# Performance work log

Measured on AMD Instinct MI355X. Metric: run time of the kernel, lower is better.

Reference implementation:

```python
import jax, jax.numpy as jnp
import numpy as np

B, C, H, W, HID = 4, 32, 256, 256, 64
EPS = 1e-5


def setup_inputs() -> dict:
    key = jax.random.key(0)
    ks = jax.random.split(key, 8)
    s = 0.05
    return {
        "x": jax.random.normal(ks[0], (B, C, H, W), jnp.float32),
        "Wqkv": jax.random.normal(ks[1], (3 * C, C), jnp.float32) * s,   # Conv2d 1x1, no bias
        "W1": jax.random.normal(ks[2], (HID, C), jnp.float32) * s,       # Linear(C -> HID)
        "b1": jnp.zeros((HID,), jnp.float32),
        "ln_w": jnp.ones((HID,), jnp.float32),
        "ln_b": jnp.zeros((HID,), jnp.float32),
        "W2": jax.random.normal(ks[3], (C, HID), jnp.float32) * s,       # Linear(HID -> C)
        "b2": jnp.zeros((C,), jnp.float32),
        "Wg": jax.random.normal(ks[4], (C, C), jnp.float32) * s,         # gate Conv2d 1x1
        "bg": jnp.zeros((C,), jnp.float32),
    }


def _unfold3x3(t):
    # t: (b, c, h, w) -> (b, c, 9, h, w), zero-padded 3x3 neighbors,
    # neighbor order matches F.unfold row-major kernel order.
    b, c, h, w = t.shape
    tp = jnp.pad(t, ((0, 0), (0, 0), (1, 1), (1, 1)))
    return jnp.stack(
        [tp[:, :, dy:dy + h, dx:dx + w] for dy in range(3) for dx in range(3)],
        axis=2,
    )


def reference(x, Wqkv, W1, b1, ln_w, ln_b, W2, b2, Wg, bg):
    b, c, h, w = x.shape
    qkv = jnp.einsum('oc,bchw->bohw', Wqkv, x)
    q, k, v = jnp.split(qkv, 3, axis=1)

    k_un = _unfold3x3(k)  # (b, c, 9, h, w)
    v_un = _unfold3x3(v)

    # (b, h, w, 9, c)
    q_minus_k = jnp.transpose(q[:, :, None] - k_un, (0, 3, 4, 2, 1))

    hid = jnp.einsum('bhwnc,dc->bhwnd', q_minus_k, W1) + b1
    mean = hid.mean(-1, keepdims=True)
    std = jnp.sqrt(((hid - mean) ** 2).mean(-1, keepdims=True))  # unbiased=False
    hid = ln_w * ((hid - mean) / (std + EPS)) + ln_b
    hid = jax.nn.relu(hid)
    scores = jnp.einsum('bhwnd,cd->bhwnc', hid, W2) + b2

    attn = jax.nn.softmax(scores, axis=-2)  # over neighbor dim (9)
    neighbors_v = jnp.transpose(v_un, (0, 3, 4, 2, 1))  # (b, h, w, 9, c)
    weighted_v = jnp.sum(neighbors_v * attn, axis=3)     # (b, h, w, c)
    weighted_v = jnp.transpose(weighted_v, (0, 3, 1, 2)) # (b, c, h, w)

    base = jnp.einsum('oc,bchw->bohw', Wg, x) + bg[None, :, None, None]
    return weighted_v + base + x
```

## Files before the change

kernel.cpp:

```cpp
#include <hip/hip_runtime.h>


#define HWm 65536
#define NPIX 262144
#define PW 258
#define PHW 66564
#define LOG2E 1.44269504088896340736f

typedef __attribute__((ext_vector_type(8))) _Float16 half8;
typedef __attribute__((ext_vector_type(2))) _Float16 half2v;
typedef __attribute__((ext_vector_type(4))) float f32x4;

__device__ __forceinline__ unsigned pkh(float a, float b) {
    auto h = __builtin_amdgcn_cvt_pkrtz(a, b);
    return __builtin_bit_cast(unsigned, h);
}
__device__ __forceinline__ half2v h2(unsigned u) { return __builtin_bit_cast(half2v, u); }
__device__ __forceinline__ unsigned u2(half2v h) { return __builtin_bit_cast(unsigned, h); }

__global__ __launch_bounds__(256) void prep_kernel(
    const float* __restrict__ Wqkv, const float* __restrict__ W1,
    const float* __restrict__ W2, const float* __restrict__ b1v,
    const float* __restrict__ Wg, const float* __restrict__ bgv,
    const float* __restrict__ lnw, const float* __restrict__ lnb,
    float* __restrict__ Wk1, float* __restrict__ Wq1,
    unsigned* __restrict__ W2A, unsigned* __restrict__ waA,
    float* __restrict__ biasF, unsigned* __restrict__ beta2G)
{
    const int tid = threadIdx.x;
    for (int i = tid; i < 2048; i += 256) {
        const int d = i >> 5, c = i & 31;
        float aq = 0.f, ak = 0.f;
#pragma unroll
        for (int k = 0; k < 32; ++k) {
            const float w1 = W1[d * 32 + k];
            aq = fmaf(w1, Wqkv[k * 32 + c], aq);
            ak = fmaf(w1, Wqkv[(32 + k) * 32 + c], ak);
        }
        Wq1[i] = aq;
        Wk1[i] = ak;
    }
    for (int i = tid; i < 1024; i += 256) {
        const int w = i & 3;
        const int lane = (i >> 2) & 63;
        const int kb = (i >> 8) & 1;
        const int ct = (i >> 9) & 1;
        const int row = (lane & 15) + 16 * ct;
        const int k0 = kb * 32 + ((lane >> 4) & 3) * 8 + 2 * w;
        const float s0 = (fabsf(lnw[k0]) < 1e-8f) ? 0.f : lnw[k0] * LOG2E;
        const float s1 = (fabsf(lnw[k0 + 1]) < 1e-8f) ? 0.f : lnw[k0 + 1] * LOG2E;
        W2A[i] = pkh(W2[row * 64 + k0] * s0, W2[row * 64 + k0 + 1] * s1);
    }
    for (int i = tid; i < 32; i += 256) {
        const float w0 = lnw[2 * i], w1 = lnw[2 * i + 1];
        const float be0 = (fabsf(w0) < 1e-8f) ? 0.f : lnb[2 * i] / w0;
        const float be1 = (fabsf(w1) < 1e-8f) ? 0.f : lnb[2 * i + 1] / w1;
        beta2G[i] = pkh(be0, be1);
    }
    __syncthreads();
    for (int i = tid; i < 3072; i += 256) {
        const int t = i >> 8;
        const int l = (i >> 2) & 63;
        const int w2 = i & 3;
        const int row = 16 * t + (l & 15);
        const int k0 = ((l >> 4) & 3) * 8 + 2 * w2;
        float a0, a1;
        if (row < 64)        { a0 = Wk1[row * 32 + k0];            a1 = Wk1[row * 32 + k0 + 1]; }
        else if (row < 128)  { a0 = Wq1[(row - 64) * 32 + k0];     a1 = Wq1[(row - 64) * 32 + k0 + 1]; }
        else if (row < 160)  { a0 = Wqkv[(row - 64) * 32 + k0];    a1 = Wqkv[(row - 64) * 32 + k0 + 1]; }
        else {
            const int gr = row - 160;
            a0 = Wg[gr * 32 + k0]     + ((gr == k0)     ? 1.f : 0.f);
            a1 = Wg[gr * 32 + k0 + 1] + ((gr == k0 + 1) ? 1.f : 0.f);
        }
        waA[i] = pkh(a0, a1);
    }
    for (int i = tid; i < 3072; i += 256) {
        const int t = i >> 8;
        const int l = (i >> 2) & 63;
        const int r = i & 3;
        const int row = 16 * t + ((l >> 4) & 3) * 4 + r;
        float bv = 0.f;
        if (row >= 64 && row < 128) bv = b1v[row - 64];
        else if (row >= 160)        bv = bgv[row - 160];
        biasF[i] = bv;
    }
}

__global__ __launch_bounds__(256) void kv_kernel(
    const float* __restrict__ x, const half8* __restrict__ waA,
    const float4* __restrict__ biasF, unsigned* __restrict__ khP,
    unsigned* __restrict__ qhg, unsigned* __restrict__ vP,
    float* __restrict__ SkP, float* __restrict__ SqG,
    float* __restrict__ out)
{
    const int bid = blockIdx.x;
    const int tid = threadIdx.x;

    if (bid >= 1024) {
        const int t = (bid - 1024) * 256 + tid;
        if (t < 4112) {
            const int bb = t / 1028;
            const int rr = t - bb * 1028;
            int hh, ww;
            if (rr < 258)      { hh = 0;             ww = rr; }
            else if (rr < 516) { hh = 257;           ww = rr - 258; }
            else if (rr < 772) { hh = rr - 516 + 1;  ww = 0; }
            else               { hh = rr - 772 + 1;  ww = 257; }
            const size_t pixP = (size_t)bb * PHW + hh * PW + ww;
            uint4* kp = (uint4*)khP + pixP * 8;
            uint4* vp = (uint4*)vP + pixP * 4;
            const uint4 z = { 0u, 0u, 0u, 0u };
#pragma unroll
            for (int i = 0; i < 8; ++i) kp[i] = z;
#pragma unroll
            for (int i = 0; i < 4; ++i) vp[i] = z;
            SkP[pixP] = 0.f;
        }
        return;
    }

    __shared__ __align__(16) unsigned xT[256 * 16];

    const int b = bid >> 8;
    const int h = bid & 255;
    const int pix0 = bid * 256;
    const int rowP0 = b * PHW + (h + 1) * PW + 1;

    {
        const float* xp = x + (size_t)b * (32 * HWm) + h * 256 + tid;
        float xv[32];
#pragma unroll
        for (int c = 0; c < 32; ++c) xv[c] = xp[c * HWm];
        unsigned* myx = &xT[tid * 16];
#pragma unroll
        for (int cc = 0; cc < 4; ++cc) {
            uint4 u;
            u.x = pkh(xv[cc * 8 + 0], xv[cc * 8 + 1]);
            u.y = pkh(xv[cc * 8 + 2], xv[cc * 8 + 3]);
            u.z = pkh(xv[cc * 8 + 4], xv[cc * 8 + 5]);
            u.w = pkh(xv[cc * 8 + 6], xv[cc * 8 + 7]);
            *(uint4*)(myx + (((cc + tid) & 3) * 4)) = u;
        }
    }

    const int l = tid & 63;
    const int wid = tid >> 6;
    const int g = l >> 4;
    const int c15 = l & 15;

    half8 A[12];
    f32x4 bF[12];
#pragma unroll
    for (int t = 0; t < 12; ++t) {
        A[t] = waA[t * 64 + l];
        const float4 bv = biasF[t * 64 + l];
        bF[t][0] = bv.x; bF[t][1] = bv.y; bF[t][2] = bv.z; bF[t][3] = bv.w;
    }

#pragma unroll
    for (int pp = 0; pp < 4; ++pp) {
        const int pg = wid * 4 + pp;
        const int px = pg * 16 + c15;
        const half8 bfrag = *(const half8*)&xT[px * 16 + (((g + px) & 3) * 4)];

        f32x4 Ct[12];
#pragma unroll
        for (int t = 0; t < 12; ++t)
            Ct[t] = __builtin_amdgcn_mfma_f32_16x16x32_f16(A[t], bfrag, bF[t], 0, 0, 0);

        const size_t pixP = (size_t)(rowP0 + px);
        const int pixg = pix0 + px;

        float sk = 0.f;
        {
            char* krec = (char*)khP + pixP * 128 + g * 8;
#pragma unroll
            for (int t = 0; t < 4; ++t) {
                uint2 uu;
                uu.x = pkh(Ct[t][0], Ct[t][1]);
                uu.y = pkh(Ct[t][2], Ct[t][3]);
                *(uint2*)(krec + t * 32) = uu;
                sk += (Ct[t][0] + Ct[t][1]) + (Ct[t][2] + Ct[t][3]);
            }
        }
        float sq = 0.f;
        {
            char* qrec = (char*)qhg + (size_t)pixg * 128 + g * 8;
#pragma unroll
            for (int t = 4; t < 8; ++t) {
                uint2 uu;
                uu.x = pkh(Ct[t][0], Ct[t][1]);
                uu.y = pkh(Ct[t][2], Ct[t][3]);
                *(uint2*)(qrec + (t - 4) * 32) = uu;
                sq += (Ct[t][0] + Ct[t][1]) + (Ct[t][2] + Ct[t][3]);
            }
        }
        {
            char* vrec = (char*)vP + pixP * 64 + g * 8;
#pragma unroll
            for (int t = 8; t < 10; ++t) {
                uint2 uu;
                uu.x = pkh(Ct[t][0], Ct[t][1]);
                uu.y = pkh(Ct[t][2], Ct[t][3]);
                *(uint2*)(vrec + (t - 8) * 32) = uu;
            }
        }
        {
            float* op = out + (size_t)b * (32 * HWm) + h * 256 + px;
#pragma unroll
            for (int t = 10; t < 12; ++t) {
#pragma unroll
                for (int r = 0; r < 4; ++r)
                    op[(16 * (t - 10) + g * 4 + r) * HWm] = Ct[t][r];
            }
        }
        sk += __shfl_xor(sk, 16);
        sk += __shfl_xor(sk, 32);
        sq += __shfl_xor(sq, 16);
        sq += __shfl_xor(sq, 32);
        if (g == 0) {
            SkP[pixP] = sk;
            SqG[pixg] = sq;
        }
    }
}

__global__ __launch_bounds__(512) void attn_kernel(
    const unsigned* __restrict__ qhg, const unsigned* __restrict__ khP,
    const unsigned* __restrict__ vP, const half8* __restrict__ w2a,
    const float* __restrict__ SkP, const float* __restrict__ SqG,
    const unsigned* __restrict__ beta2G, float* __restrict__ out)
{
    __shared__ __align__(16) char mergeL[32768];

    const int tid = threadIdx.x;
    const int grp = tid >> 8;
    const int p = tid & 255;

    const int bid = blockIdx.x;
    const int swz = (bid & 7) * 128 + (bid >> 3);
    const int b = swz >> 8;
    const int trem = swz & 255;
    const int h0 = (trem >> 4) << 4;
    const int w0 = (trem & 15) << 4;

    const int l = tid & 63;
    const int lane15 = p & 15;
    const int q = (p >> 4) & 3;
    const int wrow = (p >> 6) & 3;
    const int gRow0 = wrow * 4;

    const int pixU0 = (b << 16) + ((h0 + gRow0) << 8) + (w0 + lane15);
    const int pixP0 = b * PHW + (h0 + gRow0 + 1) * PW + (w0 + lane15 + 1);

    uint4 qf[4][2];
    float Sq4[4];
#pragma unroll
    for (int gg = 0; gg < 4; ++gg) {
        const uint4* qr = (const uint4*)qhg + (size_t)(pixU0 + gg * 256) * 8;
        qf[gg][0] = qr[q];
        qf[gg][1] = qr[4 + q];
        Sq4[gg] = SqG[pixU0 + gg * 256];
    }

    half2v bet[2][4];
#pragma unroll
    for (int j = 0; j < 4; ++j) {
        bet[0][j] = h2(beta2G[q * 4 + j]);
        bet[1][j] = h2(beta2G[(4 + q) * 4 + j]);
    }

    const half8 a00 = w2a[0 * 64 + l];
    const half8 a01 = w2a[1 * 64 + l];
    const half8 a10 = w2a[2 * 64 + l];
    const half8 a11 = w2a[3 * 64 + l];

    half2v wv2[16], ssum2[16];
    const half2v zero2 = { (_Float16)0.f, (_Float16)0.f };
#pragma unroll
    for (int i = 0; i < 16; ++i) { wv2[i] = zero2; ssum2[i] = zero2; }

    const uint4* khP4 = (const uint4*)khP;
    const int vbase0 = b * PHW + (h0 + 1) * PW + (w0 + 1) + lane15;

    const int cnt = grp ? 5 : 4;
    int relOff = grp ? 0 : (-PW - 1);
    int m3 = grp ? 1 : 0;

#pragma unroll
    for (int nn = 0; nn < 5; ++nn) {
        if (nn >= cnt) break;

        float ss[4];
        half2v hd[4][2][4];
#pragma unroll
        for (int gg = 0; gg < 4; ++gg) {
            const int nofs = pixP0 + gg * PW + relOff;
            const uint4* kr = khP4 + (size_t)nofs * 8;
            const uint4 k0 = kr[q];
            const uint4 k1 = kr[4 + q];
            hd[gg][0][0] = h2(qf[gg][0].x) - h2(k0.x);
            hd[gg][0][1] = h2(qf[gg][0].y) - h2(k0.y);
            hd[gg][0][2] = h2(qf[gg][0].z) - h2(k0.z);
            hd[gg][0][3] = h2(qf[gg][0].w) - h2(k0.w);
            hd[gg][1][0] = h2(qf[gg][1].x) - h2(k1.x);
            hd[gg][1][1] = h2(qf[gg][1].y) - h2(k1.y);
            hd[gg][1][2] = h2(qf[gg][1].z) - h2(k1.z);
            hd[gg][1][3] = h2(qf[gg][1].w) - h2(k1.w);
            float s = 0.f;
#pragma unroll
            for (int c = 0; c < 2; ++c)
#pragma unroll
                for (int j = 0; j < 4; ++j)
                    s = __builtin_amdgcn_fdot2(hd[gg][c][j], hd[gg][c][j], s, false);
            ss[gg] = s;
        }
#pragma unroll
        for (int gg = 0; gg < 4; ++gg) {
            ss[gg] += __shfl_xor(ss[gg], 16);
            ss[gg] += __shfl_xor(ss[gg], 32);
        }

#pragma unroll
        for (int gg = 0; gg < 4; ++gg) {
            const float Sk = SkP[pixP0 + gg * PW + relOff];
            const float sum = Sq4[gg] - Sk;
            const float mean = sum * 0.015625f;
            float var = fmaf(-mean, mean, ss[gg] * 0.015625f);
            var = fmaxf(var, 0.f);
            const float inv = __builtin_amdgcn_rcpf(sqrtf(var) + 1e-5f);
            const float nmi = -mean * inv;
            const half2v inv2 = { (_Float16)inv, (_Float16)inv };
            const half2v nmi2 = { (_Float16)nmi, (_Float16)nmi };

            uint4 u0, u1;
            {
                unsigned uw[2][4];
#pragma unroll
                for (int c = 0; c < 2; ++c)
#pragma unroll
                    for (int j = 0; j < 4; ++j) {
                        half2v u = __builtin_elementwise_fma(hd[gg][c][j], inv2, nmi2 + bet[c][j]);
                        u = __builtin_elementwise_max(u, zero2);
                        uw[c][j] = u2(u);
                    }
                u0.x = uw[0][0]; u0.y = uw[0][1]; u0.z = uw[0][2]; u0.w = uw[0][3];
                u1.x = uw[1][0]; u1.y = uw[1][1]; u1.z = uw[1][2]; u1.w = uw[1][3];
            }
            const half8 B0 = __builtin_bit_cast(half8, u0);
            const half8 B1 = __builtin_bit_cast(half8, u1);

            const f32x4 z4 = { 0.f, 0.f, 0.f, 0.f };
            f32x4 acc0 = __builtin_amdgcn_mfma_f32_16x16x32_f16(a00, B0, z4, 0, 0, 0);
            acc0 = __builtin_amdgcn_mfma_f32_16x16x32_f16(a01, B1, acc0, 0, 0, 0);
            f32x4 acc1 = __builtin_amdgcn_mfma_f32_16x16x32_f16(a10, B0, z4, 0, 0, 0);
            acc1 = __builtin_amdgcn_mfma_f32_16x16x32_f16(a11, B1, acc1, 0, 0, 0);

            const int npP = vbase0 + (gRow0 + gg) * PW + relOff;
            const unsigned* vp = vP + (size_t)npP * 16;
            const uint2 vA = *(const uint2*)(vp + q * 2);
            const uint2 vB = *(const uint2*)(vp + 8 + q * 2);

            const half2v e01 = h2(pkh(__builtin_amdgcn_exp2f(acc0[0]), __builtin_amdgcn_exp2f(acc0[1])));
            const half2v e23 = h2(pkh(__builtin_amdgcn_exp2f(acc0[2]), __builtin_amdgcn_exp2f(acc0[3])));
            const half2v f01 = h2(pkh(__builtin_amdgcn_exp2f(acc1[0]), __builtin_amdgcn_exp2f(acc1[1])));
            const half2v f23 = h2(pkh(__builtin_amdgcn_exp2f(acc1[2]), __builtin_amdgcn_exp2f(acc1[3])));
            ssum2[gg * 4 + 0] += e01;
            ssum2[gg * 4 + 1] += e23;
            ssum2[gg * 4 + 2] += f01;
            ssum2[gg * 4 + 3] += f23;
            wv2[gg * 4 + 0] = __builtin_elementwise_fma(e01, h2(vA.x), wv2[gg * 4 + 0]);
            wv2[gg * 4 + 1] = __builtin_elementwise_fma(e23, h2(vA.y), wv2[gg * 4 + 1]);
            wv2[gg * 4 + 2] = __builtin_elementwise_fma(f01, h2(vB.x), wv2[gg * 4 + 2]);
            wv2[gg * 4 + 3] = __builtin_elementwise_fma(f23, h2(vB.y), wv2[gg * 4 + 3]);
        }

        const int step = (m3 == 2) ? (PW - 2) : 1;
        relOff += step;
        m3 = (m3 == 2) ? 0 : m3 + 1;
    }

    __syncthreads();
    if (grp == 1) {
#pragma unroll
        for (int j4 = 0; j4 < 4; ++j4) {
            uint4 o;
            o.x = u2(wv2[j4 * 4 + 0]); o.y = u2(wv2[j4 * 4 + 1]);
            o.z = u2(wv2[j4 * 4 + 2]); o.w = u2(wv2[j4 * 4 + 3]);
            *(uint4*)(mergeL + j4 * 4096 + p * 16) = o;
        }
#pragma unroll
        for (int j4 = 0; j4 < 4; ++j4) {
            uint4 o;
            o.x = u2(ssum2[j4 * 4 + 0]); o.y = u2(ssum2[j4 * 4 + 1]);
            o.z = u2(ssum2[j4 * 4 + 2]); o.w = u2(ssum2[j4 * 4 + 3]);
            *(uint4*)(mergeL + (4 + j4) * 4096 + p * 16) = o;
        }
    }
    __syncthreads();
    if (grp == 0) {
#pragma unroll
        for (int j4 = 0; j4 < 4; ++j4) {
            const uint4 t = *(const uint4*)(mergeL + j4 * 4096 + p * 16);
            wv2[j4 * 4 + 0] += h2(t.x); wv2[j4 * 4 + 1] += h2(t.y);
            wv2[j4 * 4 + 2] += h2(t.z); wv2[j4 * 4 + 3] += h2(t.w);
        }
#pragma unroll
        for (int j4 = 0; j4 < 4; ++j4) {
            const uint4 t = *(const uint4*)(mergeL + (4 + j4) * 4096 + p * 16);
            ssum2[j4 * 4 + 0] += h2(t.x); ssum2[j4 * 4 + 1] += h2(t.y);
            ssum2[j4 * 4 + 2] += h2(t.z); ssum2[j4 * 4 + 3] += h2(t.w);
        }
#pragma unroll
        for (int gg = 0; gg < 4; ++gg) {
            const int g = gRow0 + gg;
            float* op = out + (size_t)b * (32 * HWm) + ((h0 + g) << 8) + (w0 + lane15);
#pragma unroll
            for (int r = 0; r < 4; ++r) {
                const int ch0 = q * 4 + r;
                const int ch1 = 16 + q * 4 + r;
                const float w0v = (float)((r < 2) ? wv2[gg * 4 + 0][r] : wv2[gg * 4 + 1][r - 2]);
                const float s0v = (float)((r < 2) ? ssum2[gg * 4 + 0][r] : ssum2[gg * 4 + 1][r - 2]);
                const float w1v = (float)((r < 2) ? wv2[gg * 4 + 2][r] : wv2[gg * 4 + 3][r - 2]);
                const float s1v = (float)((r < 2) ? ssum2[gg * 4 + 2][r] : ssum2[gg * 4 + 3][r - 2]);
                op[ch0 * HWm] += w0v * __builtin_amdgcn_rcpf(s0v);
                op[ch1 * HWm] += w1v * __builtin_amdgcn_rcpf(s1v);
            }
        }
    }
}

extern "C" void kernel_launch(void* const* d_in, const int* in_sizes, int n_in,
                              void* d_out, int out_size, void* d_ws, size_t ws_size,
                              hipStream_t stream) {
    const float* x    = (const float*)d_in[0];
    const float* Wqkv = (const float*)d_in[1];
    const float* W1   = (const float*)d_in[2];
    const float* b1   = (const float*)d_in[3];
    const float* lnw  = (const float*)d_in[4];
    const float* lnb  = (const float*)d_in[5];
    const float* W2   = (const float*)d_in[6];
    const float* b2   = (const float*)d_in[7];
    const float* Wg   = (const float*)d_in[8];
    const float* bg   = (const float*)d_in[9];
    float* out = (float*)d_out;
    (void)b2;

    float* ws  = (float*)d_ws;
    float* Wk1 = ws;
    float* Wq1 = ws + 2048;
    unsigned* W2A  = (unsigned*)(ws + 4096);
    unsigned* waA  = (unsigned*)(ws + 5120);
    float*    biasF = ws + 8192;
    unsigned* beta2G = (unsigned*)(ws + 11264);
    unsigned* khP = (unsigned*)(ws + 11328);
    unsigned* qhg = khP + (size_t)4 * PHW * 32;
    unsigned* vP  = qhg + (size_t)NPIX * 32;
    float* SkP = (float*)(vP + (size_t)4 * PHW * 16);
    float* SqG = SkP + (size_t)4 * PHW;

    prep_kernel<<<1, 256, 0, stream>>>(Wqkv, W1, W2, b1, Wg, bg, lnw, lnb,
                                       Wk1, Wq1, W2A, waA, biasF, beta2G);
    kv_kernel<<<1024 + 17, 256, 0, stream>>>(x, (const half8*)waA,
                                             (const float4*)biasF,
                                             khP, qhg, vP, SkP, SqG, out);
    attn_kernel<<<1024, 512, 0, stream>>>(qhg, khP, vP, (const half8*)W2A,
                                          SkP, SqG, beta2G, out);
}
```

Baseline: 121.4 us.

## Split 9-neighbor attention across four 256-thread groups with tree merge

The attention kernel grows from 512 to 1024 threads per block, so the nine neighbor taps are split across four thread groups (2,2,2,3) instead of two (4,5). Neighbor offsets become compile-time constants through a macro, and per-pixel q vectors and Sq are reloaded inside each iteration instead of being held in registers. Partial softmax numerators and denominators are combined through a two-level shared-memory reduction that now uses 64KB. This shortens each thread's serial chain and raises parallelism per tile, at the cost of an extra merge stage with a barrier, larger shared memory, redundant q loads, and possible register pressure under the 1024-thread launch bound.

Measured after the change: 223.4 us. 1.84x slower.

```diff
diff --git a/kernel.cpp b/kernel.cpp
--- a/kernel.cpp
+++ b/kernel.cpp
@@ -226,13 +226,96 @@
     }
 }
 
-__global__ __launch_bounds__(512) void attn_kernel(
+#define NB_ITER(RELC)                                                           \
+{                                                                               \
+    constexpr int relC = (RELC);                                                \
+    float ss[4];                                                                \
+    half2v hd[4][2][4];                                                         \
+    _Pragma("unroll")                                                           \
+    for (int gg = 0; gg < 4; ++gg) {                                            \
+        const uint4* kr = khP4 + (size_t)(pixB[gg] + relC) * 8;                 \
+        const uint4 k0 = kr[q];                                                 \
+        const uint4 k1 = kr[4 + q];                                             \
+        const uint4 qa = *(const uint4*)(qhg + (size_t)(pixU0 + gg * 256) * 32 + q * 4);        \
+        const uint4 qb = *(const uint4*)(qhg + (size_t)(pixU0 + gg * 256) * 32 + (4 + q) * 4);  \
+        hd[gg][0][0] = h2(qa.x) - h2(k0.x);                                     \
+        hd[gg][0][1] = h2(qa.y) - h2(k0.y);                                     \
+        hd[gg][0][2] = h2(qa.z) - h2(k0.z);                                     \
+        hd[gg][0][3] = h2(qa.w) - h2(k0.w);                                     \
+        hd[gg][1][0] = h2(qb.x) - h2(k1.x);                                     \
+        hd[gg][1][1] = h2(qb.y) - h2(k1.y);                                     \
+        hd[gg][1][2] = h2(qb.z) - h2(k1.z);                                     \
+        hd[gg][1][3] = h2(qb.w) - h2(k1.w);                                     \
+        float s = 0.f;                                                          \
+        _Pragma("unroll")                                                       \
+        for (int c = 0; c < 2; ++c)                                             \
+            _Pragma("unroll")                                                   \
+            for (int j = 0; j < 4; ++j)                                         \
+                s = __builtin_amdgcn_fdot2(hd[gg][c][j], hd[gg][c][j], s, false); \
+        ss[gg] = s;                                                             \
+    }                                                                           \
+    _Pragma("unroll")                                                           \
+    for (int gg = 0; gg < 4; ++gg) {                                            \
+        ss[gg] += __shfl_xor(ss[gg], 16);                                       \
+        ss[gg] += __shfl_xor(ss[gg], 32);                                       \
+    }                                                                           \
+    _Pragma("unroll")                                                           \
+    for (int gg = 0; gg < 4; ++gg) {                                            \
+        const float Sk = SkP[pixB[gg] + relC];                                  \
+        const float sum = SqG[pixU0 + gg * 256] - Sk;                           \
+        const float mean = sum * 0.015625f;                                     \
+        float var = fmaf(-mean, mean, ss[gg] * 0.015625f);                      \
+        var = fmaxf(var, 0.f);                                                  \
+        const float inv = __builtin_amdgcn_rcpf(sqrtf(var) + 1e-5f);            \
+        const float nmi = -mean * inv;                                          \
+        const half2v inv2 = { (_Float16)inv, (_Float16)inv };                   \
+        const half2v nmi2 = { (_Float16)nmi, (_Float16)nmi };                   \
+        uint4 u0, u1;                                                           \
+        {                                                                       \
+            unsigned uw[2][4];                                                  \
+            _Pragma("unroll")                                                   \
+            for (int c = 0; c < 2; ++c)                                         \
+                _Pragma("unroll")                                               \
+                for (int j = 0; j < 4; ++j) {                                   \
+                    half2v u = __builtin_elementwise_fma(hd[gg][c][j], inv2, nmi2 + bet[c][j]); \
+                    u = __builtin_elementwise_max(u, zero2);                    \
+                    uw[c][j] = u2(u);                                           \
+                }                                                               \
+            u0.x = uw[0][0]; u0.y = uw[0][1]; u0.z = uw[0][2]; u0.w = uw[0][3]; \
+            u1.x = uw[1][0]; u1.y = uw[1][1]; u1.z = uw[1][2]; u1.w = uw[1][3]; \
+        }                                                                       \
+        const half8 B0 = __builtin_bit_cast(half8, u0);                         \
+        const half8 B1 = __builtin_bit_cast(half8, u1);                         \
+        const f32x4 z4 = { 0.f, 0.f, 0.f, 0.f };                                \
+        f32x4 acc0 = __builtin_amdgcn_mfma_f32_16x16x32_f16(a00, B0, z4, 0, 0, 0); \
+        acc0 = __builtin_amdgcn_mfma_f32_16x16x32_f16(a01, B1, acc0, 0, 0, 0);  \
+        f32x4 acc1 = __builtin_amdgcn_mfma_f32_16x16x32_f16(a10, B0, z4, 0, 0, 0); \
+        acc1 = __builtin_amdgcn_mfma_f32_16x16x32_f16(a11, B1, acc1, 0, 0, 0);  \
+        const unsigned* vp = vP + (size_t)(pixB[gg] + relC) * 16;               \
+        const uint2 vA = *(const uint2*)(vp + q * 2);                           \
+        const uint2 vB4 = *(const uint2*)(vp + 8 + q * 2);                      \
+        const half2v e01 = h2(pkh(__builtin_amdgcn_exp2f(acc0[0]), __builtin_amdgcn_exp2f(acc0[1]))); \
+        const half2v e23 = h2(pkh(__builtin_amdgcn_exp2f(acc0[2]), __builtin_amdgcn_exp2f(acc0[3]))); \
+        const half2v f01 = h2(pkh(__builtin_amdgcn_exp2f(acc1[0]), __builtin_amdgcn_exp2f(acc1[1]))); \
+        const half2v f23 = h2(pkh(__builtin_amdgcn_exp2f(acc1[2]), __builtin_amdgcn_exp2f(acc1[3]))); \
+        ssum2[gg * 4 + 0] += e01;                                               \
+        ssum2[gg * 4 + 1] += e23;                                               \
+        ssum2[gg * 4 + 2] += f01;                                               \
+        ssum2[gg * 4 + 3] += f23;                                               \
+        wv2[gg * 4 + 0] = __builtin_elementwise_fma(e01, h2(vA.x), wv2[gg * 4 + 0]);  \
+        wv2[gg * 4 + 1] = __builtin_elementwise_fma(e23, h2(vA.y), wv2[gg * 4 + 1]);  \
+        wv2[gg * 4 + 2] = __builtin_elementwise_fma(f01, h2(vB4.x), wv2[gg * 4 + 2]); \
+        wv2[gg * 4 + 3] = __builtin_elementwise_fma(f23, h2(vB4.y), wv2[gg * 4 + 3]); \
+    }                                                                           \
+}
+
+__global__ __launch_bounds__(1024) void attn_kernel(
     const unsigned* __restrict__ qhg, const unsigned* __restrict__ khP,
     const unsigned* __restrict__ vP, const half8* __restrict__ w2a,
     const float* __restrict__ SkP, const float* __restrict__ SqG,
     const unsigned* __restrict__ beta2G, float* __restrict__ out)
 {
-    __shared__ __align__(16) char mergeL[32768];
+    __shared__ __align__(16) char mergeL[65536];
 
     const int tid = threadIdx.x;
     const int grp = tid >> 8;
@@ -252,17 +335,10 @@
     const int gRow0 = wrow * 4;
 
     const int pixU0 = (b << 16) + ((h0 + gRow0) << 8) + (w0 + lane15);
-    const int pixP0 = b * PHW + (h0 + gRow0 + 1) * PW + (w0 + lane15 + 1);
-
-    uint4 qf[4][2];
-    float Sq4[4];
-#pragma unroll
-    for (int gg = 0; gg < 4; ++gg) {
-        const uint4* qr = (const uint4*)qhg + (size_t)(pixU0 + gg * 256) * 8;
-        qf[gg][0] = qr[q];
-        qf[gg][1] = qr[4 + q];
-        Sq4[gg] = SqG[pixU0 + gg * 256];
-    }
+    int pixB[4];
+#pragma unroll
+    for (int gg = 0; gg < 4; ++gg)
+        pixB[gg] = b * PHW + (h0 + gRow0 + gg + 1) * PW + (w0 + lane15 + 1);
 
     half2v bet[2][4];
 #pragma unroll
@@ -282,107 +358,48 @@
     for (int i = 0; i < 16; ++i) { wv2[i] = zero2; ssum2[i] = zero2; }
 
     const uint4* khP4 = (const uint4*)khP;
-    const int vbase0 = b * PHW + (h0 + 1) * PW + (w0 + 1) + lane15;
-
-    const int cnt = grp ? 5 : 4;
-    int relOff = grp ? 0 : (-PW - 1);
-    int m3 = grp ? 1 : 0;
-
-#pragma unroll
-    for (int nn = 0; nn < 5; ++nn) {
-        if (nn >= cnt) break;
-
-        float ss[4];
-        half2v hd[4][2][4];
-#pragma unroll
-        for (int gg = 0; gg < 4; ++gg) {
-            const int nofs = pixP0 + gg * PW + relOff;
-            const uint4* kr = khP4 + (size_t)nofs * 8;
-            const uint4 k0 = kr[q];
-            const uint4 k1 = kr[4 + q];
-            hd[gg][0][0] = h2(qf[gg][0].x) - h2(k0.x);
-            hd[gg][0][1] = h2(qf[gg][0].y) - h2(k0.y);
-            hd[gg][0][2] = h2(qf[gg][0].z) - h2(k0.z);
-            hd[gg][0][3] = h2(qf[gg][0].w) - h2(k0.w);
-            hd[gg][1][0] = h2(qf[gg][1].x) - h2(k1.x);
-            hd[gg][1][1] = h2(qf[gg][1].y) - h2(k1.y);
-            hd[gg][1][2] = h2(qf[gg][1].z) - h2(k1.z);
-            hd[gg][1][3] = h2(qf[gg][1].w) - h2(k1.w);
-            float s = 0.f;
-#pragma unroll
-            for (int c = 0; c < 2; ++c)
-#pragma unroll
-                for (int j = 0; j < 4; ++j)
-                    s = __builtin_amdgcn_fdot2(hd[gg][c][j], hd[gg][c][j], s, false);
-            ss[gg] = s;
-        }
-#pragma unroll
-        for (int gg = 0; gg < 4; ++gg) {
-            ss[gg] += __shfl_xor(ss[gg], 16);
-            ss[gg] += __shfl_xor(ss[gg], 32);
-        }
-
-#pragma unroll
-        for (int gg = 0; gg < 4; ++gg) {
-            const float Sk = SkP[pixP0 + gg * PW + relOff];
-            const float sum = Sq4[gg] - Sk;
-            const float mean = sum * 0.015625f;
-            float var = fmaf(-mean, mean, ss[gg] * 0.015625f);
-            var = fmaxf(var, 0.f);
-            const float inv = __builtin_amdgcn_rcpf(sqrtf(var) + 1e-5f);
-            const float nmi = -mean * inv;
-            const half2v inv2 = { (_Float16)inv, (_Float16)inv };
-            const half2v nmi2 = { (_Float16)nmi, (_Float16)nmi };
-
-            uint4 u0, u1;
-            {
-                unsigned uw[2][4];
-#pragma unroll
-                for (int c = 0; c < 2; ++c)
-#pragma unroll
-                    for (int j = 0; j < 4; ++j) {
-                        half2v u = __builtin_elementwise_fma(hd[gg][c][j], inv2, nmi2 + bet[c][j]);
-                        u = __builtin_elementwise_max(u, zero2);
-                        uw[c][j] = u2(u);
-                    }
-                u0.x = uw[0][0]; u0.y = uw[0][1]; u0.z = uw[0][2]; u0.w = uw[0][3];
-                u1.x = uw[1][0]; u1.y = uw[1][1]; u1.z = uw[1][2]; u1.w = uw[1][3];
-            }
-            const half8 B0 = __builtin_bit_cast(half8, u0);
-            const half8 B1 = __builtin_bit_cast(half8, u1);
-
-            const f32x4 z4 = { 0.f, 0.f, 0.f, 0.f };
-            f32x4 acc0 = __builtin_amdgcn_mfma_f32_16x16x32_f16(a00, B0, z4, 0, 0, 0);
-            acc0 = __builtin_amdgcn_mfma_f32_16x16x32_f16(a01, B1, acc0, 0, 0, 0);
-            f32x4 acc1 = __builtin_amdgcn_mfma_f32_16x16x32_f16(a10, B0, z4, 0, 0, 0);
-            acc1 = __builtin_amdgcn_mfma_f32_16x16x32_f16(a11, B1, acc1, 0, 0, 0);
-
-            const int npP = vbase0 + (gRow0 + gg) * PW + relOff;
-            const unsigned* vp = vP + (size_t)npP * 16;
-            const uint2 vA = *(const uint2*)(vp + q * 2);
-            const uint2 vB = *(const uint2*)(vp + 8 + q * 2);
-
-            const half2v e01 = h2(pkh(__builtin_amdgcn_exp2f(acc0[0]), __builtin_amdgcn_exp2f(acc0[1])));
-            const half2v e23 = h2(pkh(__builtin_amdgcn_exp2f(acc0[2]), __builtin_amdgcn_exp2f(acc0[3])));
-            const half2v f01 = h2(pkh(__builtin_amdgcn_exp2f(acc1[0]), __builtin_amdgcn_exp2f(acc1[1])));
-            const half2v f23 = h2(pkh(__builtin_amdgcn_exp2f(acc1[2]), __builtin_amdgcn_exp2f(acc1[3])));
-            ssum2[gg * 4 + 0] += e01;
-            ssum2[gg * 4 + 1] += e23;
-            ssum2[gg * 4 + 2] += f01;
-            ssum2[gg * 4 + 3] += f23;
-            wv2[gg * 4 + 0] = __builtin_elementwise_fma(e01, h2(vA.x), wv2[gg * 4 + 0]);
-            wv2[gg * 4 + 1] = __builtin_elementwise_fma(e23, h2(vA.y), wv2[gg * 4 + 1]);
-            wv2[gg * 4 + 2] = __builtin_elementwise_fma(f01, h2(vB.x), wv2[gg * 4 + 2]);
-            wv2[gg * 4 + 3] = __builtin_elementwise_fma(f23, h2(vB.y), wv2[gg * 4 + 3]);
-        }
-
-        const int step = (m3 == 2) ? (PW - 2) : 1;
-        relOff += step;
-        m3 = (m3 == 2) ? 0 : m3 + 1;
-    }
+
+    if (grp == 0)      { NB_ITER(-PW - 1) NB_ITER(-PW) }
+    else if (grp == 1) { NB_ITER(-PW + 1) NB_ITER(-1) }
+    else if (grp == 2) { NB_ITER(0)       NB_ITER(1) }
+    else               { NB_ITER(PW - 1)  NB_ITER(PW) NB_ITER(PW + 1) }
 
     __syncthreads();
-    if (grp == 1) {
+    if (grp == 1 || grp == 3) {
+        char* base = mergeL + ((grp == 3) ? 32768 : 0);
+#pragma unroll
+        for (int j4 = 0; j4 < 4; ++j4) {
+            uint4 o;
+            o.x = u2(wv2[j4 * 4 + 0]); o.y = u2(wv2[j4 * 4 + 1]);
+            o.z = u2(wv2[j4 * 4 + 2]); o.w = u2(wv2[j4 * 4 + 3]);
+            *(uint4*)(base + j4 * 4096 + p * 16) = o;
+        }
+#pragma unroll
+        for (int j4 = 0; j4 < 4; ++j4) {
+            uint4 o;
+            o.x = u2(ssum2[j4 * 4 + 0]); o.y = u2(ssum2[j4 * 4 + 1]);
+            o.z = u2(ssum2[j4 * 4 + 2]); o.w = u2(ssum2[j4 * 4 + 3]);
+            *(uint4*)(base + (4 + j4) * 4096 + p * 16) = o;
+        }
+    }
+    __syncthreads();
+    if (grp == 0 || grp == 2) {
+        const char* base = mergeL + ((grp == 2) ? 32768 : 0);
+#pragma unroll
+        for (int j4 = 0; j4 < 4; ++j4) {
+            const uint4 t = *(const uint4*)(base + j4 * 4096 + p * 16);
+            wv2[j4 * 4 + 0] += h2(t.x); wv2[j4 * 4 + 1] += h2(t.y);
+            wv2[j4 * 4 + 2] += h2(t.z); wv2[j4 * 4 + 3] += h2(t.w);
+        }
+#pragma unroll
+        for (int j4 = 0; j4 < 4; ++j4) {
+            const uint4 t = *(const uint4*)(base + (4 + j4) * 4096 + p * 16);
+            ssum2[j4 * 4 + 0] += h2(t.x); ssum2[j4 * 4 + 1] += h2(t.y);
+            ssum2[j4 * 4 + 2] += h2(t.z); ssum2[j4 * 4 + 3] += h2(t.w);
+        }
+    }
+    __syncthreads();
+    if (grp == 2) {
 #pragma unroll
         for (int j4 = 0; j4 < 4; ++j4) {
             uint4 o;
@@ -465,6 +482,6 @@
     kv_kernel<<<1024 + 17, 256, 0, stream>>>(x, (const half8*)waA,
                                              (const float4*)biasF,
                                              khP, qhg, vP, SkP, SqG, out);
-    attn_kernel<<<1024, 512, 0, stream>>>(qhg, khP, vP, (const half8*)W2A,
-                                          SkP, SqG, beta2G, out);
-}
+    attn_kernel<<<1024, 1024, 0, stream>>>(qhg, khP, vP, (const half8*)W2A,
+                                           SkP, SqG, beta2G, out);
+}
```
